# Optimization experiments

Hardware: AMD Instinct MI355X
Metric: run time of the kernel (lower is better)

## Reference

```python
import jax, jax.numpy as jnp
import numpy as np

N_FREQ = 5
K = 16  # nneigh


def _gather(points, idx):
    # points: [B,N,C], idx: [B,nQ,K] -> [B,nQ,K,C]
    return jax.vmap(lambda p, i: p[i])(points, idx)


def setup_inputs() -> dict:
    key = jax.random.key(0)
    ks = jax.random.split(key, 16)
    B, nQ, N, dim_inp, dim = 2, 8192, 4096, 128, 128
    s = dim_inp ** -0.5
    return {
        "xyz_q": jax.random.uniform(ks[0], (B, nQ, 2), jnp.float32),
        "lat_rep": jax.random.normal(ks[1], (B, dim_inp), jnp.float32),
        "xyz": jax.random.uniform(ks[2], (B, N, 3), jnp.float32),
        "points": jax.random.normal(ks[3], (B, N, dim_inp), jnp.float32),
        "w_qs": jax.random.normal(ks[4], (dim_inp, dim), jnp.float32) * s,
        "w_ks": jax.random.normal(ks[5], (dim_inp, dim), jnp.float32) * s,
        "w_vs": jax.random.normal(ks[6], (dim_inp, dim), jnp.float32) * s,
        "w_kg": jax.random.normal(ks[7], (dim_inp, dim), jnp.float32) * s,
        "w_vg": jax.random.normal(ks[8], (dim_inp, dim), jnp.float32) * s,
        "gamma_w1": jax.random.normal(ks[9], (dim, dim), jnp.float32) * (dim ** -0.5),
        "gamma_b1": jnp.zeros((dim,), jnp.float32),
        "gamma_w2": jax.random.normal(ks[10], (dim, dim), jnp.float32) * (dim ** -0.5),
        "gamma_b2": jnp.zeros((dim,), jnp.float32),
        "pe_w": jax.random.normal(ks[11], (3 * 2 * N_FREQ + 3, dim), jnp.float32) * (33 ** -0.5),
        "pe_b": jnp.zeros((dim,), jnp.float32),
    }


def reference(xyz_q, lat_rep, xyz, points, w_qs, w_ks, w_vs, w_kg, w_vg,
              gamma_w1, gamma_b1, gamma_w2, gamma_b2, pe_w, pe_b):
    b, nQ, _ = xyz_q.shape
    dim = w_qs.shape[1]
    # kNN in 2D (no_grad in original): squared distance [B,nQ,N]
    dists = jnp.sum((xyz_q[:, :, None] - xyz[:, None, :, :2]) ** 2, axis=-1)
    _, knn_idx = jax.lax.top_k(-dists, K)  # ascending distance order

    # global latent [B,dim_inp] branch
    q_attn = (lat_rep @ w_qs)[:, None, None, :]          # [B,1,1,dim]
    k_global = jnp.broadcast_to((lat_rep @ w_kg)[:, None, None, :], (b, nQ, 1, dim))
    v_global = jnp.broadcast_to((lat_rep @ w_vg)[:, None, None, :], (b, nQ, 1, dim))

    k_attn = jnp.concatenate([_gather(points @ w_ks, knn_idx), k_global], axis=2)  # [B,nQ,K+1,dim]
    v_attn = jnp.concatenate([_gather(points @ w_vs, knn_idx), v_global], axis=2)

    xyz_knn = _gather(xyz, knn_idx)                      # [B,nQ,K,3]
    pos_diff = jnp.concatenate(
        [xyz_q[:, :, None] - xyz_knn[..., :2], xyz_knn[..., -1:]], axis=-1)  # [B,nQ,K,3]
    freq_bands = jnp.linspace(1.0, 2.0 ** N_FREQ, N_FREQ)
    embeds = [pos_diff]
    for fr in freq_bands:
        embeds.append(jnp.sin(pos_diff * fr))
        embeds.append(jnp.cos(pos_diff * fr))
    pos_embed = jnp.concatenate(embeds, axis=-1)         # [B,nQ,K,33]
    pos_encode = pos_embed @ pe_w + pe_b                 # [B,nQ,K,dim]
    pos_encode = jnp.concatenate(
        [pos_encode, jnp.zeros((b, nQ, 1, dim), pos_encode.dtype)], axis=2)  # [B,nQ,K+1,dim]

    h = q_attn - k_attn + pos_encode
    h = jnp.maximum(h @ gamma_w1 + gamma_b1, 0.0) @ gamma_w2 + gamma_b2
    attn = jax.nn.softmax(h, axis=-2)                    # softmax over neighbor axis
    res = jnp.sum(attn * (v_attn + pos_encode), axis=2)  # einsum 'bmnf,bmnf->bmf'
    return res
```

## Files before the change

### kernel.cpp

```cpp
#include <hip/hip_runtime.h>
#include <cstdint>

#define DIM   128
#define KNN   16
#define NB    2
#define NQ    8192
#define NPTS  4096
#define KVROWS 16
#define GRID  32
#define NCELL (GRID*GRID)
#define CAP   384

typedef unsigned short ushort_t;
typedef short vshort8 __attribute__((ext_vector_type(8)));
typedef float vfloat4 __attribute__((ext_vector_type(4)));

__device__ __forceinline__ ushort_t bf16_rne(float f) {
    unsigned u = __float_as_uint(f);
    unsigned r = u + 0x7FFFu + ((u >> 16) & 1u);
    return (ushort_t)(r >> 16);
}
__device__ __forceinline__ int cell_of(float x) {
    int c = (int)(x * 32.0f);
    return min(max(c, 0), GRID - 1);
}
__device__ __forceinline__ float f4_at(float4 v, int i) {
    return (i == 0) ? v.x : (i == 1) ? v.y : (i == 2) ? v.z : v.w;
}

__device__ __forceinline__ void pack_body(
    const float* __restrict__ src, int K, int ncols, int NT, int KS,
    ushort_t* __restrict__ dst, int gid)
{
    int total = NT*KS*64;
    if (gid >= total) return;
    int lane = gid & 63; int c = gid >> 6;
    int s = c % KS; int n = c / KS;
    int k0 = s*32 + ((lane >> 4) << 3);
    int col = n*16 + (lane & 15);
    vshort8 v;
    #pragma unroll
    for (int i = 0; i < 8; ++i) {
        int k = k0 + i;
        float f = (k < K) ? src[k*ncols + col] : 0.f;
        v[i] = (short)bf16_rne(f);
    }
    *(vshort8*)(dst + gid*8) = v;
}

__device__ __forceinline__ void scan1024(
    const int* __restrict__ cnt, int* __restrict__ cs, int* __restrict__ cu,
    int* __restrict__ ss, int t)
{
    int v0 = cnt[t*4 + 0];
    int v1 = cnt[t*4 + 1];
    int v2 = cnt[t*4 + 2];
    int v3 = cnt[t*4 + 3];
    int p0 = v0, p1 = p0 + v1, p2 = p1 + v2, p3 = p2 + v3;
    ss[t] = p3;
    __syncthreads();
    for (int off = 1; off < 256; off <<= 1) {
        int add = (t >= off) ? ss[t - off] : 0;
        __syncthreads();
        ss[t] += add;
        __syncthreads();
    }
    int excl = ss[t] - p3;
    cs[t*4 + 0] = excl;        cu[t*4 + 0] = excl;
    cs[t*4 + 1] = excl + p0;   cu[t*4 + 1] = excl + p0;
    cs[t*4 + 2] = excl + p1;   cu[t*4 + 2] = excl + p1;
    cs[t*4 + 3] = excl + p2;   cu[t*4 + 3] = excl + p2;
    if (t == 255) cs[NCELL] = ss[255];
}

__global__ __launch_bounds__(256) void pre1_k(
    const float* __restrict__ w_ks, const float* __restrict__ g_w1,
    const float* __restrict__ pe_w, const float* __restrict__ xyz,
    const float* __restrict__ xyz_q,
    float* __restrict__ Wk1, float* __restrict__ pwc,
    int* __restrict__ cellcnt, int* __restrict__ qcnt)
{
    int t = threadIdx.x; int bx = blockIdx.x;
    if (bx < 64) {
        int row = bx*2 + (t >> 7); int f = t & 127;
        float acc = 0.f;
        for (int c = 0; c < 128; ++c) acc = fmaf(w_ks[row*128 + c], g_w1[c*128 + f], acc);
        Wk1[row*128 + f] = acc;
    } else if (bx < 128) {
        int r = bx - 64; int col = t;
        float v = 0.f;
        if (r < 33) {
            if (col < 128) {
                float a = 0.f;
                for (int c = 0; c < 128; ++c) a = fmaf(pe_w[r*128 + c], g_w1[c*128 + col], a);
                v = a;
            } else {
                v = pe_w[r*128 + (col - 128)];
            }
        }
        pwc[r*256 + col] = v;
    } else if (bx < 160) {
        int gid = (bx - 128)*256 + t;
        int b = gid >> 12; int n = gid & (NPTS - 1);
        const float* p = xyz + (b*NPTS + n)*3;
        atomicAdd(&cellcnt[b*NCELL + cell_of(p[1])*GRID + cell_of(p[0])], 1);
    } else {
        int gid = (bx - 160)*256 + t;
        int b = gid >> 13; int q = gid & (NQ - 1);
        const float* p = xyz_q + (b*NQ + q)*2;
        atomicAdd(&qcnt[b*NCELL + cell_of(p[1])*GRID + cell_of(p[0])], 1);
    }
}

__global__ __launch_bounds__(256) void pre2_k(
    const float* __restrict__ pwc, const float* __restrict__ g_w2,
    const int* __restrict__ cnt, const int* __restrict__ qcnt,
    const float* __restrict__ lat, const float* __restrict__ w_qs,
    const float* __restrict__ w_kg, const float* __restrict__ w_vg,
    const float* __restrict__ g_w1, const float* __restrict__ g_b1,
    const float* __restrict__ pe_b,
    ushort_t* __restrict__ pwf, ushort_t* __restrict__ w2f,
    int* __restrict__ cell_start, int* __restrict__ cursor,
    int* __restrict__ qstart, int* __restrict__ qcursor,
    float* __restrict__ c1_out, float* __restrict__ vg_out, float* __restrict__ h2g_out)
{
    __shared__ int ss[256];
    __shared__ float qs[NB][DIM];
    __shared__ float hgx[NB][DIM];
    __shared__ float h1gx[NB][DIM];
    int t = threadIdx.x; int bx = blockIdx.x;
    if (bx < 4) {
        pack_body(pwc, 32, 256, 16, 1, pwf, bx*256 + t);
    } else if (bx < 12) {
        pack_body(g_w2, 128, 128, 8, 4, w2f, (bx - 4)*256 + t);
    } else if (bx < 14) {
        int b = bx - 12;
        scan1024(cnt + b*NCELL, cell_start + b*(NCELL+1), cursor + b*NCELL, ss, t);
    } else if (bx < 16) {
        int b = bx - 14;
        scan1024(qcnt + b*NCELL, qstart + b*(NCELL+1), qcursor + b*NCELL, ss, t);
    } else {
        int b = t >> 7; int f = t & 127;
        float aq = 0.f, ak = 0.f, av = 0.f;
        for (int c = 0; c < DIM; ++c) {
            float l = lat[b*DIM + c];
            aq = fmaf(l, w_qs[c*DIM + f], aq);
            ak = fmaf(l, w_kg[c*DIM + f], ak);
            av = fmaf(l, w_vg[c*DIM + f], av);
        }
        vg_out[b*DIM + f] = av;
        qs[b][f] = aq + pe_b[f];
        hgx[b][f] = aq - ak;
        __syncthreads();
        float acc = g_b1[f], acch = g_b1[f];
        for (int c = 0; c < DIM; ++c) {
            float w = g_w1[c*DIM + f];
            acc  = fmaf(qs[b][c], w, acc);
            acch = fmaf(hgx[b][c], w, acch);
        }
        c1_out[b*DIM + f] = acc;
        h1gx[b][f] = fmaxf(acch, 0.f);
        __syncthreads();
        float acc2 = 0.f;
        for (int c = 0; c < DIM; ++c) acc2 = fmaf(h1gx[b][c], g_w2[c*DIM + f], acc2);
        h2g_out[b*DIM + f] = acc2;
    }
}

__global__ __launch_bounds__(256) void pre3_k(
    const float* __restrict__ points, const float* __restrict__ Wk1,
    const float* __restrict__ w_vs, const float* __restrict__ pe_b,
    const float* __restrict__ c1_,
    const float* __restrict__ xyz, const float* __restrict__ xyz_q,
    int* __restrict__ cursor, int* __restrict__ qcursor,
    float* __restrict__ K1c, float* __restrict__ Vp,
    float2* __restrict__ sxy, int* __restrict__ sidx,
    float2* __restrict__ qsxy, int* __restrict__ qsidx)
{
    __shared__ __align__(16) float pts[KVROWS*DIM];
    int t = threadIdx.x; int bx = blockIdx.x;
    if (bx < 512) {
        int r0 = bx * KVROWS;
        int b = r0 >> 12;
        #pragma unroll
        for (int k = 0; k < KVROWS*DIM/256; ++k) {
            int e = t + k*256;
            pts[e] = points[r0*DIM + e];
        }
        __syncthreads();
        int f = t & 127; int mat = t >> 7;
        const float* W = mat ? w_vs : Wk1;
        float* O = mat ? Vp : K1c;
        float addv = mat ? pe_b[f] : c1_[b*DIM + f];
        float sgn  = mat ? 1.f : -1.f;
        int fc = (f & 15)*8 + (f >> 4);
        float acc[KVROWS];
        #pragma unroll
        for (int r = 0; r < KVROWS; ++r) acc[r] = 0.f;
        const float4* pts4 = reinterpret_cast<const float4*>(pts);
        for (int c4 = 0; c4 < DIM/4; ++c4) {
            float w0 = W[(c4*4+0)*DIM + f];
            float w1 = W[(c4*4+1)*DIM + f];
            float w2 = W[(c4*4+2)*DIM + f];
            float w3 = W[(c4*4+3)*DIM + f];
            #pragma unroll
            for (int r = 0; r < KVROWS; ++r) {
                float4 p = pts4[r*(DIM/4) + c4];
                acc[r] = fmaf(p.x, w0, acc[r]);
                acc[r] = fmaf(p.y, w1, acc[r]);
                acc[r] = fmaf(p.z, w2, acc[r]);
                acc[r] = fmaf(p.w, w3, acc[r]);
            }
        }
        #pragma unroll
        for (int r = 0; r < KVROWS; ++r) O[(r0 + r)*DIM + fc] = fmaf(sgn, acc[r], addv);
    } else if (bx < 544) {
        int gid = (bx - 512)*256 + t;
        int b = gid >> 12; int n = gid & (NPTS - 1);
        const float* p = xyz + (b*NPTS + n)*3;
        float x = p[0], y = p[1];
        int slot = atomicAdd(&cursor[b*NCELL + cell_of(y)*GRID + cell_of(x)], 1);
        sxy[b*NPTS + slot] = make_float2(x, y);
        sidx[b*NPTS + slot] = n;
    } else {
        int gid = (bx - 544)*256 + t;
        int b = gid >> 13; int q = gid & (NQ - 1);
        const float* p = xyz_q + (b*NQ + q)*2;
        float x = p[0], y = p[1];
        int slot = atomicAdd(&qcursor[b*NCELL + cell_of(y)*GRID + cell_of(x)], 1);
        qsxy[b*NQ + slot] = make_float2(x, y);
        qsidx[b*NQ + slot] = q;
    }
}

__global__ __launch_bounds__(256) void knn_k(
    const float2* __restrict__ qsxy, const float2* __restrict__ sxy,
    const int* __restrict__ sidx, const int* __restrict__ cstart,
    int* __restrict__ knn_out)
{
    __shared__ float cand_d[4][CAP];
    __shared__ int   cand_i[4][CAP];
    int t = threadIdx.x; int wid = t >> 6, lane = t & 63;
    int bx = blockIdx.x; int b = bx >> 11; int q = (bx & 2047)*4 + wid;
    float2 qp = qsxy[b*NQ + q];
    float xq = qp.x, yq = qp.y;
    int cx = cell_of(xq), cy = cell_of(yq);
    const int* cs_b = cstart + b*(NCELL+1);
    float* cd = cand_d[wid]; int* ci = cand_i[wid];
    const float INF = 3.4e38f;
    const float CS = 1.0f/32.0f;
    int* outp = knn_out + (b*NQ + q)*KNN;
    unsigned long long lmask = (1ull << lane) - 1ull;

    for (int R = 2; R < 9; ++R) {
        int x0 = max(cx-R, 0), x1 = min(cx+R, GRID-1);
        int y0 = max(cy-R, 0), y1 = min(cy+R, GRID-1);
        int cnt = 0;
        for (int ry = y0; ry <= y1; ++ry) {
            int s0 = cs_b[ry*GRID + x0];
            int e0 = cs_b[ry*GRID + x1 + 1];
            for (int o = s0 + lane; o < e0; o += 64) {
                float2 p = sxy[b*NPTS + o];
                float dx = __fadd_rn(xq, -p.x);
                float dy = __fadd_rn(yq, -p.y);
                float d = __fadd_rn(__fmul_rn(dx, dx), __fmul_rn(dy, dy));
                int slot = cnt + (o - s0);
                if (slot < CAP) { cd[slot] = d; ci[slot] = o; }
            }
            cnt += e0 - s0;
        }
        asm volatile("s_waitcnt lgkmcnt(0)" ::: "memory");
        __builtin_amdgcn_sched_barrier(0);

        int cc = min(cnt, CAP);
        float dr[6];
        #pragma unroll
        for (int k = 0; k < 6; ++k)
            dr[k] = (lane + k*64 < cc) ? cd[lane + k*64] : INF;

        unsigned lo = 0u, hi = 0x40000000u;
        #pragma unroll 1
        for (int it = 0; it < 32; ++it) {
            if (hi - lo <= 1u) break;
            unsigned mid = (lo + hi) >> 1;
            float pv = __uint_as_float(mid);
            int c = 0;
            #pragma unroll
            for (int k = 0; k < 6; ++k)
                c += __popcll(__ballot(dr[k] <= pv));
            if (c >= KNN) {
                hi = mid;
                if (c == KNN) break;
            } else {
                lo = mid;
            }
        }
        float thr = __uint_as_float(hi);

        float bl = (x0 > 0)      ? (xq - (float)x0*CS)       : INF;
        float br = (x1 < GRID-1) ? ((float)(x1+1)*CS - xq)   : INF;
        float bb = (y0 > 0)      ? (yq - (float)y0*CS)       : INF;
        float bt = (y1 < GRID-1) ? ((float)(y1+1)*CS - yq)   : INF;
        float safe = fminf(fminf(bl, br), fminf(bb, bt)) - 2e-6f;
        bool whole = (safe > 1e8f);
        bool ok = (cnt >= KNN) && (cnt <= CAP) && (whole || thr <= safe*safe);
        if (ok || R == 8) {
            int base = 0;
            #pragma unroll
            for (int k = 0; k < 6; ++k) {
                bool p = dr[k] < thr;
                unsigned long long m = __ballot(p);
                int pos = base + __popcll(m & lmask);
                if (p && pos < KNN) outp[pos] = sidx[b*NPTS + ci[lane + k*64]];
                base += __popcll(m);
            }
            #pragma unroll
            for (int k = 0; k < 6; ++k) {
                bool p = dr[k] == thr;
                unsigned long long m = __ballot(p);
                int pos = base + __popcll(m & lmask);
                if (p && pos < KNN) outp[pos] = sidx[b*NPTS + ci[lane + k*64]];
                base += __popcll(m);
            }
            break;
        }
    }
}

__global__ __launch_bounds__(512, 2) void fuse_k(
    const float2* __restrict__ qsxy, const int* __restrict__ qsidx,
    const float* __restrict__ xyz,
    const float* __restrict__ K1c, const float* __restrict__ Vp,
    const int* __restrict__ knn_idx,
    const float* __restrict__ vg_, const float* __restrict__ h2g_,
    const float* __restrict__ pw32_,
    const ushort_t* __restrict__ pwf, const ushort_t* __restrict__ w2f,
    float* __restrict__ out)
{
    __shared__ __align__(16) ushort_t w2B[32*512];
    __shared__ __align__(16) ushort_t h1b[8][2048];

    int t = threadIdx.x, lane = t & 63, wid = t >> 6;
    int sid = (blockIdx.x & 7) * 64 + (blockIdx.x >> 3);
    int b = sid >> 8; int qbase = (sid & 255) * 32;

    {
        const int4* s2 = (const int4*)w2f;  int4* d2 = (int4*)w2B;
        #pragma unroll
        for (int i = 0; i < 4; ++i) d2[t + i*512] = s2[t + i*512];
    }
    __syncthreads();

    int c16 = lane & 15, g = lane >> 4, rowbase = g*4;
    ushort_t* hb = h1b[wid];
    const vshort8* pwBv = (const vshort8*)pwf;
    const vshort8* w2Bv = (const vshort8*)w2B;
    const float4* K4 = (const float4*)K1c;
    const float4* V4 = (const float4*)Vp;
    const vfloat4 vzero = (vfloat4){0.f, 0.f, 0.f, 0.f};

    float pw32r[16], hgr[8], vgr[8];
    #pragma unroll
    for (int n = 0; n < 16; ++n) pw32r[n] = pw32_[n*16 + c16];
    #pragma unroll
    for (int n = 0; n < 8; ++n) {
        hgr[n] = h2g_[b*128 + n*16 + c16];
        vgr[n] = vg_[b*128 + n*16 + c16];
    }

    #pragma unroll 1
    for (int qi = 0; qi < 4; ++qi) {
        int q = qbase + wid*4 + qi;
        float2 qp = qsxy[b*NQ + q];
        float xq = qp.x, yq = qp.y;
        int qorig = qsidx[b*NQ + q];
        int idxrow = knn_idx[(b*NQ + q)*KNN + c16];
        const float* p = xyz + (b*NPTS + idxrow)*3;
        float pd0 = xq - p[0], pd1 = yq - p[1], pd2 = p[2];
        int rf4[4];
        #pragma unroll
        for (int r = 0; r < 4; ++r)
            rf4[r] = (b*NPTS + __shfl(idxrow, rowbase + r))*32 + c16*2;

        vshort8 eh;
        int k0 = g*8;
        #pragma unroll
        for (int j = 0; j < 8; ++j) {
            int k = k0 + j;
            float v;
            if (k < 3) {
                v = (k == 0) ? pd0 : (k == 1 ? pd1 : pd2);
            } else {
                int m = k - 3; int fi = m / 6; int rem = m - fi*6;
                int comp = (rem < 3) ? rem : rem - 3;
                float pdc = (comp == 0) ? pd0 : (comp == 1 ? pd1 : pd2);
                float fr = (fi == 0) ? 1.0f : (fi == 1) ? 8.75f : (fi == 2) ? 16.5f
                         : (fi == 3) ? 24.25f : 32.0f;
                float arg = pdc * fr;
                v = (rem < 3) ? __sinf(arg) : __cosf(arg);
            }
            eh[j] = (short)bf16_rne(v);
        }
        float c32 = __cosf(32.0f * pd2);
        float c32r[4];
        #pragma unroll
        for (int r = 0; r < 4; ++r) c32r[r] = __shfl(c32, rowbase + r);

        #pragma unroll
        for (int half = 0; half < 2; ++half) {
            float4 k1q[4];
            #pragma unroll
            for (int r = 0; r < 4; ++r) k1q[r] = K4[rf4[r] + half];
            #pragma unroll
            for (int nn = 0; nn < 4; ++nn) {
                int n = half*4 + nn;
                vfloat4 a = __builtin_amdgcn_mfma_f32_16x16x32_bf16(
                    eh, pwBv[n*64 + lane], vzero, 0, 0, 0);
                int col = n*16 + c16;
                int s = col >> 5;
                int lp = ((col >> 3) & 3) << 4;
                int j = c16 & 7;
                #pragma unroll
                for (int r = 0; r < 4; ++r) {
                    float h = f4_at(k1q[r], nn) + fmaf(c32r[r], pw32r[n], a[r]);
                    h = fmaxf(h, 0.f);
                    hb[s*512 + (lp | (rowbase + r))*8 + j] = bf16_rne(h);
                }
            }
        }
        asm volatile("s_waitcnt lgkmcnt(0)" ::: "memory");
        __builtin_amdgcn_sched_barrier(0);

        vfloat4 acc2[8];
        #pragma unroll
        for (int n = 0; n < 8; ++n) acc2[n] = vzero;
        #pragma unroll
        for (int s = 0; s < 4; ++s) {
            vshort8 ah = ((const vshort8*)hb)[s*64 + lane];
            #pragma unroll
            for (int n = 0; n < 8; ++n) {
                vshort8 bh = w2Bv[(n*4 + s)*64 + lane];
                acc2[n] = __builtin_amdgcn_mfma_f32_16x16x32_bf16(ah, bh, acc2[n], 0, 0, 0);
            }
        }

        #pragma unroll
        for (int half = 0; half < 2; ++half) {
            float4 vq[4];
            #pragma unroll
            for (int r = 0; r < 4; ++r) vq[r] = V4[rf4[r] + half];
            #pragma unroll
            for (int nn = 0; nn < 4; ++nn) {
                int n = half*4 + nn;
                vfloat4 ap = __builtin_amdgcn_mfma_f32_16x16x32_bf16(
                    eh, pwBv[(8 + n)*64 + lane], vzero, 0, 0, 0);
                #pragma unroll
                for (int r = 0; r < 4; ++r) ap[r] = fmaf(c32r[r], pw32r[8 + n], ap[r]);

                float hg = hgr[n];
                vfloat4 a2 = acc2[n];
                float mx = fmaxf(fmaxf(a2[0], a2[1]), fmaxf(a2[2], a2[3]));
                mx = fmaxf(mx, __shfl_xor(mx, 16));
                mx = fmaxf(mx, __shfl_xor(mx, 32));
                mx = fmaxf(mx, hg);
                float sum = 0.f, num = 0.f;
                #pragma unroll
                for (int r = 0; r < 4; ++r) {
                    float ev = __expf(a2[r] - mx);
                    float v = f4_at(vq[r], nn) + ap[r];
                    sum += ev;
                    num = fmaf(ev, v, num);
                }
                sum += __shfl_xor(sum, 16); sum += __shfl_xor(sum, 32);
                num += __shfl_xor(num, 16); num += __shfl_xor(num, 32);
                float eg = __expf(hg - mx);
                sum += eg;
                num = fmaf(eg, vgr[n], num);
                if (g == 0) out[(b*NQ + qorig)*128 + n*16 + c16] = num / sum;
            }
        }
    }
}

extern "C" void kernel_launch(void* const* d_in, const int* in_sizes, int n_in,
                              void* d_out, int out_size, void* d_ws, size_t ws_size,
                              hipStream_t stream) {
    const float* xyz_q  = (const float*)d_in[0];
    const float* lat    = (const float*)d_in[1];
    const float* xyz    = (const float*)d_in[2];
    const float* points = (const float*)d_in[3];
    const float* w_qs   = (const float*)d_in[4];
    const float* w_ks   = (const float*)d_in[5];
    const float* w_vs   = (const float*)d_in[6];
    const float* w_kg   = (const float*)d_in[7];
    const float* w_vg   = (const float*)d_in[8];
    const float* g_w1   = (const float*)d_in[9];
    const float* g_b1   = (const float*)d_in[10];
    const float* g_w2   = (const float*)d_in[11];
    const float* g_b2   = (const float*)d_in[12];
    const float* pe_w   = (const float*)d_in[13];
    const float* pe_b   = (const float*)d_in[14];
    float* out = (float*)d_out;
    (void)g_b2;

    float* ws   = (float*)d_ws;
    float* Vp   = ws;
    float* K1c  = Vp  + NB*NPTS*DIM;
    float* Wk1  = K1c + NB*NPTS*DIM;
    float* pwc  = Wk1 + DIM*DIM;
    float* c1   = pwc + 64*256;
    float* vg   = c1  + NB*DIM;
    float* h2g  = vg  + NB*DIM;
    int*   knn  = (int*)(h2g + NB*DIM);
    ushort_t* pwf = (ushort_t*)(knn + NB*NQ*KNN);
    ushort_t* w2f = pwf + 16*64*8;
    int* cellcnt  = (int*)(w2f + 32*64*8);
    int* qcnt     = cellcnt + NB*NCELL;
    int* cellstart = qcnt + NB*NCELL;
    int* cursor    = cellstart + NB*(NCELL+1);
    int* qstart    = cursor + NB*NCELL;
    int* qcursor   = qstart + NB*(NCELL+1);
    int* sidx      = qcursor + NB*NCELL;
    float2* sxy    = (float2*)(sidx + NB*NPTS);
    int* qsidx     = (int*)(sxy + NB*NPTS);
    float2* qsxy   = (float2*)(qsidx + NB*NQ);

    hipMemsetAsync(cellcnt, 0, 2*NB*NCELL*sizeof(int), stream);
    pre1_k<<<224, 256, 0, stream>>>(w_ks, g_w1, pe_w, xyz, xyz_q,
                                    Wk1, pwc, cellcnt, qcnt);
    pre2_k<<<17, 256, 0, stream>>>(pwc, g_w2, cellcnt, qcnt,
                                   lat, w_qs, w_kg, w_vg, g_w1, g_b1, pe_b,
                                   pwf, w2f, cellstart, cursor, qstart, qcursor,
                                   c1, vg, h2g);
    pre3_k<<<608, 256, 0, stream>>>(points, Wk1, w_vs, pe_b, c1, xyz, xyz_q,
                                    cursor, qcursor, K1c, Vp, sxy, sidx, qsxy, qsidx);
    knn_k<<<NB*NQ/4, 256, 0, stream>>>(qsxy, sxy, sidx, cellstart, knn);
    fuse_k<<<NB*NQ/32, 512, 0, stream>>>(qsxy, qsidx, xyz, K1c, Vp, knn, vg, h2g,
                                         pwc + 32*256, pwf, w2f, out);
}
```

Before: 110.9 us.

## Move K/V projection into kNN kernel to overlap with grid scatter

Splits the old pre3 kernel so the small grid-scatter blocks run alone in a tiny kernel. The K/V projection blocks are merged into the kNN kernel as extra leading blocks, sharing one shared-memory buffer. The aim is for the compute-heavy projection to overlap with the kNN search instead of serialising before it. Shared-memory use per block grows to the kNN size for the projection blocks, which may affect occupancy.

```diff
diff --git a/kernel.cpp b/kernel.cpp
--- a/kernel.cpp
+++ b/kernel.cpp
@@ -168,18 +168,45 @@
 }
 
 __global__ __launch_bounds__(256) void pre3_k(
+    const float* __restrict__ xyz, const float* __restrict__ xyz_q,
+    int* __restrict__ cursor, int* __restrict__ qcursor,
+    float2* __restrict__ sxy, int* __restrict__ sidx,
+    float2* __restrict__ qsxy, int* __restrict__ qsidx)
+{
+    int t = threadIdx.x; int bx = blockIdx.x;
+    if (bx < 32) {
+        int gid = bx*256 + t;
+        int b = gid >> 12; int n = gid & (NPTS - 1);
+        const float* p = xyz + (b*NPTS + n)*3;
+        float x = p[0], y = p[1];
+        int slot = atomicAdd(&cursor[b*NCELL + cell_of(y)*GRID + cell_of(x)], 1);
+        sxy[b*NPTS + slot] = make_float2(x, y);
+        sidx[b*NPTS + slot] = n;
+    } else {
+        int gid = (bx - 32)*256 + t;
+        int b = gid >> 13; int q = gid & (NQ - 1);
+        const float* p = xyz_q + (b*NQ + q)*2;
+        float x = p[0], y = p[1];
+        int slot = atomicAdd(&qcursor[b*NCELL + cell_of(y)*GRID + cell_of(x)], 1);
+        qsxy[b*NQ + slot] = make_float2(x, y);
+        qsidx[b*NQ + slot] = q;
+    }
+}
+
+__global__ __launch_bounds__(256) void knnkv_k(
     const float* __restrict__ points, const float* __restrict__ Wk1,
     const float* __restrict__ w_vs, const float* __restrict__ pe_b,
     const float* __restrict__ c1_,
-    const float* __restrict__ xyz, const float* __restrict__ xyz_q,
-    int* __restrict__ cursor, int* __restrict__ qcursor,
+    const float2* __restrict__ qsxy, const float2* __restrict__ sxy,
+    const int* __restrict__ sidx, const int* __restrict__ cstart,
     float* __restrict__ K1c, float* __restrict__ Vp,
-    float2* __restrict__ sxy, int* __restrict__ sidx,
-    float2* __restrict__ qsxy, int* __restrict__ qsidx)
-{
-    __shared__ __align__(16) float pts[KVROWS*DIM];
+    int* __restrict__ knn_out)
+{
+    __shared__ __align__(16) float smem[4*CAP*2];
     int t = threadIdx.x; int bx = blockIdx.x;
+
     if (bx < 512) {
+        float* pts = smem;
         int r0 = bx * KVROWS;
         int b = r0 >> 12;
         #pragma unroll
@@ -214,39 +241,18 @@
         }
         #pragma unroll
         for (int r = 0; r < KVROWS; ++r) O[(r0 + r)*DIM + fc] = fmaf(sgn, acc[r], addv);
-    } else if (bx < 544) {
-        int gid = (bx - 512)*256 + t;
-        int b = gid >> 12; int n = gid & (NPTS - 1);
-        const float* p = xyz + (b*NPTS + n)*3;
-        float x = p[0], y = p[1];
-        int slot = atomicAdd(&cursor[b*NCELL + cell_of(y)*GRID + cell_of(x)], 1);
-        sxy[b*NPTS + slot] = make_float2(x, y);
-        sidx[b*NPTS + slot] = n;
-    } else {
-        int gid = (bx - 544)*256 + t;
-        int b = gid >> 13; int q = gid & (NQ - 1);
-        const float* p = xyz_q + (b*NQ + q)*2;
-        float x = p[0], y = p[1];
-        int slot = atomicAdd(&qcursor[b*NCELL + cell_of(y)*GRID + cell_of(x)], 1);
-        qsxy[b*NQ + slot] = make_float2(x, y);
-        qsidx[b*NQ + slot] = q;
-    }
-}
-
-__global__ __launch_bounds__(256) void knn_k(
-    const float2* __restrict__ qsxy, const float2* __restrict__ sxy,
-    const int* __restrict__ sidx, const int* __restrict__ cstart,
-    int* __restrict__ knn_out)
-{
-    __shared__ float cand_d[4][CAP];
-    __shared__ int   cand_i[4][CAP];
-    int t = threadIdx.x; int wid = t >> 6, lane = t & 63;
-    int bx = blockIdx.x; int b = bx >> 11; int q = (bx & 2047)*4 + wid;
+        return;
+    }
+
+    int bxk = bx - 512;
+    int wid = t >> 6, lane = t & 63;
+    int b = bxk >> 11; int q = (bxk & 2047)*4 + wid;
+    float* cd = smem + wid*CAP;
+    int*   ci = (int*)(smem + 4*CAP) + wid*CAP;
     float2 qp = qsxy[b*NQ + q];
     float xq = qp.x, yq = qp.y;
     int cx = cell_of(xq), cy = cell_of(yq);
     const int* cs_b = cstart + b*(NCELL+1);
-    float* cd = cand_d[wid]; int* ci = cand_i[wid];
     const float INF = 3.4e38f;
     const float CS = 1.0f/32.0f;
     int* outp = knn_out + (b*NQ + q)*KNN;
@@ -532,9 +538,11 @@
                                    lat, w_qs, w_kg, w_vg, g_w1, g_b1, pe_b,
                                    pwf, w2f, cellstart, cursor, qstart, qcursor,
                                    c1, vg, h2g);
-    pre3_k<<<608, 256, 0, stream>>>(points, Wk1, w_vs, pe_b, c1, xyz, xyz_q,
-                                    cursor, qcursor, K1c, Vp, sxy, sidx, qsxy, qsidx);
-    knn_k<<<NB*NQ/4, 256, 0, stream>>>(qsxy, sxy, sidx, cellstart, knn);
+    pre3_k<<<96, 256, 0, stream>>>(xyz, xyz_q, cursor, qcursor,
+                                   sxy, sidx, qsxy, qsidx);
+    knnkv_k<<<512 + NB*NQ/4, 256, 0, stream>>>(points, Wk1, w_vs, pe_b, c1,
+                                               qsxy, sxy, sidx, cellstart,
+                                               K1c, Vp, knn);
     fuse_k<<<NB*NQ/32, 512, 0, stream>>>(qsxy, qsidx, xyz, K1c, Vp, knn, vg, h2g,
                                          pwc + 32*256, pwf, w2f, out);
 }
```

Result: no change. 111.9 us (+0.9%).
